# Performance work log

Hardware: AMD Instinct MI355X
Metric: run time of the kernel (lower is better)

## Reference

```python
import jax, jax.numpy as jnp
import numpy as np
import math

B, P = 4096, 512
WDT = 10          # lyr_wdt = number of irreps (multiplicity)
EPS2 = 1e-12      # NormActivation epsilon=1e-6, squared


def setup_inputs() -> dict:
    key = jax.random.key(0)
    ks = jax.random.split(key, 8)
    return {
        "invar_2b": jax.random.normal(ks[0], (B, P, 5), jnp.float32),
        "vectors_2b": jax.random.normal(ks[1], (B, P, 9), jnp.float32),
        # torch.nn.Linear params (stored as [in, out])
        "w1_0": jax.random.normal(ks[2], (5, WDT), jnp.float32) / math.sqrt(5.0),
        "b1_0": jnp.zeros((WDT,), jnp.float32),
        "w1_1": jax.random.normal(ks[3], (WDT, WDT), jnp.float32) / math.sqrt(float(WDT)),
        "b1_1": jnp.zeros((WDT,), jnp.float32),
        # o3.Linear weights (N(0,1) init, e3nn normalizes by sqrt(mul_in) in forward)
        "lin0_w": jax.random.normal(ks[4], (3, WDT), jnp.float32),
        "na0_b": jnp.zeros((WDT,), jnp.float32),   # NormActivation bias
        "lin1_w": jax.random.normal(ks[5], (WDT, WDT), jnp.float32),
        "na1_b": jnp.zeros((WDT,), jnp.float32),
        "final_w": jax.random.normal(ks[6], (WDT, 1), jnp.float32),
    }


def _self_intrc(x, w, bias):
    """o3.Linear (mul_in x 1o -> mul_out x 1o) + NormActivation(tanh, eps=1e-6, bias).

    x: [B, P, mul_in, 3]
    """
    mul_in = x.shape[-2]
    # single l=1 -> l=1 path; e3nn o3.Linear scales by 1/sqrt(fan_in)
    y = jnp.einsum('bpuc,uw->bpwc', x, w) / jnp.sqrt(jnp.float32(mul_in))
    # NormActivation: norm per irrep, clamped at eps^2 before sqrt
    n = jnp.sqrt(jnp.maximum(jnp.sum(y * y, axis=-1), EPS2))  # [B,P,mul_out]
    s = jnp.tanh(n + bias) / n                                # act(norm+b)/norm
    return y * s[..., None]


def reference(invar_2b, vectors_2b, w1_0, b1_0, w1_1, b1_1,
              lin0_w, na0_b, lin1_w, na1_b, final_w):
    # scalar branch: Linear(5,10) + ReLU, Linear(10,10) + ReLU
    y = jax.nn.relu(invar_2b @ w1_0 + b1_0)
    y = jax.nn.relu(y @ w1_1 + b1_1)              # [B, P, WDT] (10x0e)

    # equivariant branch: two self_intrc blocks on 3x1o -> 10x1o -> 10x1o
    v = vectors_2b.reshape(B, P, 3, 3)            # [B,P,3 irreps,3 comps]
    x = _self_intrc(v, lin0_w, na0_b)             # [B,P,WDT,3]
    x = _self_intrc(x, lin1_w, na1_b)             # [B,P,WDT,3]

    # ElementwiseTensorProduct(10x0e, 10x1o) -> 10x1o: per-irrep scalar gating
    x = y[..., None] * x                          # [B,P,WDT,3]

    # final o3.Linear 10x1o -> 1x1o
    x = jnp.einsum('bpuc,uw->bpwc', x, final_w) / jnp.sqrt(jnp.float32(WDT))
    return jnp.sum(x[..., 0, :], axis=1)          # sum over pairs -> [B, 3]
```

## Files before the change

kernel.cpp:

```cpp
#include <hip/hip_runtime.h>
#include <math.h>

#define BB 4096
#define PP 512
#define WDT 10

typedef float float2v __attribute__((ext_vector_type(2)));
typedef float float4v __attribute__((ext_vector_type(4)));

#define PKFMA(a, b, c) __builtin_elementwise_fma(a, b, c)
#define PKMAX(a, b)    __builtin_elementwise_max(a, b)

__device__ __forceinline__ float2v bc2(float s) { return (float2v){s, s}; }

__device__ __forceinline__ float fast_tanh(float x) {
    float e = __builtin_amdgcn_exp2f(x * 2.8853900817779268f);
    return 1.0f - 2.0f * __builtin_amdgcn_rcpf(e + 1.0f);
}

__global__ __launch_bounds__(512, 2) void frc_2b_kernel(
    const float* __restrict__ invar,
    const float* __restrict__ vectors,
    const float* __restrict__ w1_0,
    const float* __restrict__ b1_0,
    const float* __restrict__ w1_1,
    const float* __restrict__ b1_1,
    const float* __restrict__ lin0_w,
    const float* __restrict__ na0_b,
    const float* __restrict__ lin1_w,
    const float* __restrict__ na1_b,
    const float* __restrict__ final_w,
    float* __restrict__ out)
{
    __shared__ __align__(16) float wl[528];
    __shared__ float red[8][3];

    const int b   = blockIdx.x;
    const int tid = threadIdx.x;

    for (int t = tid; t < 528; t += 512) {
        float val = 0.f;
        if (t < 80) {
            int i = t >> 4, j = t & 15;
            if (j < WDT) val = w1_0[i * WDT + j];
        } else if (t < 240) {
            int u = t - 80, i = u >> 4, j = u & 15;
            if (j < WDT) val = w1_1[i * WDT + j];
        } else if (t < 288) {
            int u = t - 240, i = u >> 4, j = u & 15;
            if (j < WDT) val = lin0_w[i * WDT + j];
        } else if (t < 448) {
            int u = t - 288, i = u >> 4, j = u & 15;
            if (j < WDT) val = lin1_w[i * WDT + j];
        } else if (t < 464) {
            int u = t - 448; if (u < WDT) val = b1_0[u];
        } else if (t < 480) {
            int u = t - 464; if (u < WDT) val = b1_1[u];
        } else if (t < 496) {
            int u = t - 480; if (u < WDT) val = na0_b[u];
        } else if (t < 512) {
            int u = t - 496; if (u < WDT) val = na1_b[u];
        } else {
            int u = t - 512; if (u < WDT) val = final_w[u] * 0.31622776601683794f;
        }
        wl[t] = val;
    }

    const float* iv = invar   + ((size_t)b * PP + tid) * 5;
    const float* vv = vectors + ((size_t)b * PP + tid) * 9;
    float in5a[5];
    #pragma unroll
    for (int i = 0; i < 5; ++i) in5a[i] = iv[i];
    float v[9];
    #pragma unroll
    for (int i = 0; i < 9; ++i) v[i] = vv[i];

    __syncthreads();

    const float k3sq  = 0.33333333333333333f;
    const float k3k10 = 0.18257418583505536f;
    const float2v z2  = {0.f, 0.f};

    float2v yp[5];
    #pragma unroll
    for (int jp = 0; jp < 5; ++jp) yp[jp] = *(const float2v*)(wl + 448 + 2 * jp);
    #pragma unroll
    for (int i = 0; i < 5; ++i) {
        const float* r = wl + i * 16;
        float4v w03 = *(const float4v*)(r);
        float4v w47 = *(const float4v*)(r + 4);
        float2v w89 = *(const float2v*)(r + 8);
        float2v xb  = bc2(in5a[i]);
        yp[0] = PKFMA(__builtin_shufflevector(w03, w03, 0, 1), xb, yp[0]);
        yp[1] = PKFMA(__builtin_shufflevector(w03, w03, 2, 3), xb, yp[1]);
        yp[2] = PKFMA(__builtin_shufflevector(w47, w47, 0, 1), xb, yp[2]);
        yp[3] = PKFMA(__builtin_shufflevector(w47, w47, 2, 3), xb, yp[3]);
        yp[4] = PKFMA(w89, xb, yp[4]);
    }
    #pragma unroll
    for (int jp = 0; jp < 5; ++jp) yp[jp] = PKMAX(yp[jp], z2);

    float2v y2p[5];
    #pragma unroll
    for (int jp = 0; jp < 5; ++jp) y2p[jp] = *(const float2v*)(wl + 464 + 2 * jp);
    #pragma unroll
    for (int k = 0; k < WDT; ++k) {
        const float* r = wl + 80 + k * 16;
        float4v w03 = *(const float4v*)(r);
        float4v w47 = *(const float4v*)(r + 4);
        float2v w89 = *(const float2v*)(r + 8);
        float2v xb  = bc2(yp[k >> 1][k & 1]);
        y2p[0] = PKFMA(__builtin_shufflevector(w03, w03, 0, 1), xb, y2p[0]);
        y2p[1] = PKFMA(__builtin_shufflevector(w03, w03, 2, 3), xb, y2p[1]);
        y2p[2] = PKFMA(__builtin_shufflevector(w47, w47, 0, 1), xb, y2p[2]);
        y2p[3] = PKFMA(__builtin_shufflevector(w47, w47, 2, 3), xb, y2p[3]);
        y2p[4] = PKFMA(w89, xb, y2p[4]);
    }
    #pragma unroll
    for (int jp = 0; jp < 5; ++jp) y2p[jp] = PKMAX(y2p[jp], z2);

    float2v c0p[5], c1p[5], c2p[5];
    #pragma unroll
    for (int jp = 0; jp < 5; ++jp) { c0p[jp] = z2; c1p[jp] = z2; c2p[jp] = z2; }
    #pragma unroll
    for (int u = 0; u < 3; ++u) {
        const float* r = wl + 240 + u * 16;
        float4v w03 = *(const float4v*)(r);
        float4v w47 = *(const float4v*)(r + 4);
        float2v w89 = *(const float2v*)(r + 8);
        float2v wp[5] = {__builtin_shufflevector(w03, w03, 0, 1),
                         __builtin_shufflevector(w03, w03, 2, 3),
                         __builtin_shufflevector(w47, w47, 0, 1),
                         __builtin_shufflevector(w47, w47, 2, 3),
                         w89};
        float2v b0 = bc2(v[u * 3 + 0]), b1 = bc2(v[u * 3 + 1]), b2 = bc2(v[u * 3 + 2]);
        #pragma unroll
        for (int jp = 0; jp < 5; ++jp) {
            c0p[jp] = PKFMA(wp[jp], b0, c0p[jp]);
            c1p[jp] = PKFMA(wp[jp], b1, c1p[jp]);
            c2p[jp] = PKFMA(wp[jp], b2, c2p[jp]);
        }
    }
    float2v x0p[5], x1p[5], x2p[5];
    #pragma unroll
    for (int jp = 0; jp < 5; ++jp) {
        float2v n2p = PKFMA(c0p[jp], c0p[jp], PKFMA(c1p[jp], c1p[jp], c2p[jp] * c2p[jp]));
        float2v mp  = PKMAX(n2p * bc2(k3sq), bc2(1e-12f));
        float2v nab = *(const float2v*)(wl + 480 + 2 * jp);
        float fh[2];
        #pragma unroll
        for (int h = 0; h < 2; ++h) {
            float m     = mp[h];
            float inv_n = __builtin_amdgcn_rsqf(m);
            float n     = m * inv_n;
            float t     = fast_tanh(n + nab[h]);
            fh[h] = t * inv_n * k3k10;
        }
        float2v fp = {fh[0], fh[1]};
        x0p[jp] = c0p[jp] * fp;
        x1p[jp] = c1p[jp] * fp;
        x2p[jp] = c2p[jp] * fp;
    }

    float2v e0p[5], e1p[5], e2p[5];
    #pragma unroll
    for (int jp = 0; jp < 5; ++jp) { e0p[jp] = z2; e1p[jp] = z2; e2p[jp] = z2; }
    #pragma unroll
    for (int u = 0; u < WDT; ++u) {
        const float* r = wl + 288 + u * 16;
        float4v w03 = *(const float4v*)(r);
        float4v w47 = *(const float4v*)(r + 4);
        float2v w89 = *(const float2v*)(r + 8);
        float2v wp[5] = {__builtin_shufflevector(w03, w03, 0, 1),
                         __builtin_shufflevector(w03, w03, 2, 3),
                         __builtin_shufflevector(w47, w47, 0, 1),
                         __builtin_shufflevector(w47, w47, 2, 3),
                         w89};
        float2v b0 = bc2(x0p[u >> 1][u & 1]);
        float2v b1 = bc2(x1p[u >> 1][u & 1]);
        float2v b2 = bc2(x2p[u >> 1][u & 1]);
        #pragma unroll
        for (int jp = 0; jp < 5; ++jp) {
            e0p[jp] = PKFMA(wp[jp], b0, e0p[jp]);
            e1p[jp] = PKFMA(wp[jp], b1, e1p[jp]);
            e2p[jp] = PKFMA(wp[jp], b2, e2p[jp]);
        }
    }
    float2v a0p = z2, a1p = z2, a2p = z2;
    #pragma unroll
    for (int jp = 0; jp < 5; ++jp) {
        float2v n2p = PKFMA(e0p[jp], e0p[jp], PKFMA(e1p[jp], e1p[jp], e2p[jp] * e2p[jp]));
        float2v mp  = PKMAX(n2p, bc2(1e-12f));
        float2v nab = *(const float2v*)(wl + 496 + 2 * jp);
        float2v fwp = *(const float2v*)(wl + 512 + 2 * jp);
        float gh[2];
        #pragma unroll
        for (int h = 0; h < 2; ++h) {
            float m     = mp[h];
            float inv_n = __builtin_amdgcn_rsqf(m);
            float n     = m * inv_n;
            float t     = fast_tanh(n + nab[h]);
            gh[h] = y2p[jp][h] * t * inv_n * fwp[h];
        }
        float2v gp = {gh[0], gh[1]};
        a0p = PKFMA(e0p[jp], gp, a0p);
        a1p = PKFMA(e1p[jp], gp, a1p);
        a2p = PKFMA(e2p[jp], gp, a2p);
    }
    float acc0 = a0p[0] + a0p[1];
    float acc1 = a1p[0] + a1p[1];
    float acc2 = a2p[0] + a2p[1];

    #pragma unroll
    for (int off = 32; off > 0; off >>= 1) {
        acc0 += __shfl_down(acc0, off, 64);
        acc1 += __shfl_down(acc1, off, 64);
        acc2 += __shfl_down(acc2, off, 64);
    }
    const int wave = tid >> 6;
    if ((tid & 63) == 0) { red[wave][0] = acc0; red[wave][1] = acc1; red[wave][2] = acc2; }
    __syncthreads();
    if (tid == 0) {
        float r0 = 0.f, r1 = 0.f, r2 = 0.f;
        #pragma unroll
        for (int wv = 0; wv < 8; ++wv) { r0 += red[wv][0]; r1 += red[wv][1]; r2 += red[wv][2]; }
        out[b * 3 + 0] = r0;
        out[b * 3 + 1] = r1;
        out[b * 3 + 2] = r2;
    }
}

extern "C" void kernel_launch(void* const* d_in, const int* in_sizes, int n_in,
                              void* d_out, int out_size, void* d_ws, size_t ws_size,
                              hipStream_t stream) {
    const float* invar   = (const float*)d_in[0];
    const float* vectors = (const float*)d_in[1];
    const float* w1_0    = (const float*)d_in[2];
    const float* b1_0    = (const float*)d_in[3];
    const float* w1_1    = (const float*)d_in[4];
    const float* b1_1    = (const float*)d_in[5];
    const float* lin0_w  = (const float*)d_in[6];
    const float* na0_b   = (const float*)d_in[7];
    const float* lin1_w  = (const float*)d_in[8];
    const float* na1_b   = (const float*)d_in[9];
    const float* final_w = (const float*)d_in[10];
    float* out = (float*)d_out;

    frc_2b_kernel<<<BB, 512, 0, stream>>>(invar, vectors, w1_0, b1_0, w1_1, b1_1,
                                          lin0_w, na0_b, lin1_w, na1_b, final_w, out);
}
```

Baseline: 173.6 us.

## Read weights directly from global memory instead of staging them in LDS

```diff
diff --git a/kernel.cpp b/kernel.cpp
--- a/kernel.cpp
+++ b/kernel.cpp
@@ -6,10 +6,10 @@
 #define WDT 10
 
 typedef float float2v __attribute__((ext_vector_type(2)));
-typedef float float4v __attribute__((ext_vector_type(4)));
 
 #define PKFMA(a, b, c) __builtin_elementwise_fma(a, b, c)
 #define PKMAX(a, b)    __builtin_elementwise_max(a, b)
+#define FENCE()        __builtin_amdgcn_sched_barrier(0)
 
 __device__ __forceinline__ float2v bc2(float s) { return (float2v){s, s}; }
 
@@ -18,7 +18,7 @@
     return 1.0f - 2.0f * __builtin_amdgcn_rcpf(e + 1.0f);
 }
 
-__global__ __launch_bounds__(512, 2) void frc_2b_kernel(
+__global__ __launch_bounds__(512) void frc_2b_kernel(
     const float* __restrict__ invar,
     const float* __restrict__ vectors,
     const float* __restrict__ w1_0,
@@ -32,39 +32,10 @@
     const float* __restrict__ final_w,
     float* __restrict__ out)
 {
-    __shared__ __align__(16) float wl[528];
     __shared__ float red[8][3];
 
     const int b   = blockIdx.x;
     const int tid = threadIdx.x;
-
-    for (int t = tid; t < 528; t += 512) {
-        float val = 0.f;
-        if (t < 80) {
-            int i = t >> 4, j = t & 15;
-            if (j < WDT) val = w1_0[i * WDT + j];
-        } else if (t < 240) {
-            int u = t - 80, i = u >> 4, j = u & 15;
-            if (j < WDT) val = w1_1[i * WDT + j];
-        } else if (t < 288) {
-            int u = t - 240, i = u >> 4, j = u & 15;
-            if (j < WDT) val = lin0_w[i * WDT + j];
-        } else if (t < 448) {
-            int u = t - 288, i = u >> 4, j = u & 15;
-            if (j < WDT) val = lin1_w[i * WDT + j];
-        } else if (t < 464) {
-            int u = t - 448; if (u < WDT) val = b1_0[u];
-        } else if (t < 480) {
-            int u = t - 464; if (u < WDT) val = b1_1[u];
-        } else if (t < 496) {
-            int u = t - 480; if (u < WDT) val = na0_b[u];
-        } else if (t < 512) {
-            int u = t - 496; if (u < WDT) val = na1_b[u];
-        } else {
-            int u = t - 512; if (u < WDT) val = final_w[u] * 0.31622776601683794f;
-        }
-        wl[t] = val;
-    }
 
     const float* iv = invar   + ((size_t)b * PP + tid) * 5;
     const float* vv = vectors + ((size_t)b * PP + tid) * 9;
@@ -75,70 +46,67 @@
     #pragma unroll
     for (int i = 0; i < 9; ++i) v[i] = vv[i];
 
-    __syncthreads();
-
     const float k3sq  = 0.33333333333333333f;
     const float k3k10 = 0.18257418583505536f;
+    const float k10   = 0.31622776601683794f;
     const float2v z2  = {0.f, 0.f};
 
     float2v yp[5];
     #pragma unroll
-    for (int jp = 0; jp < 5; ++jp) yp[jp] = *(const float2v*)(wl + 448 + 2 * jp);
+    for (int jp = 0; jp < 5; ++jp) yp[jp] = *(const float2v*)(b1_0 + 2 * jp);
     #pragma unroll
     for (int i = 0; i < 5; ++i) {
-        const float* r = wl + i * 16;
-        float4v w03 = *(const float4v*)(r);
-        float4v w47 = *(const float4v*)(r + 4);
-        float2v w89 = *(const float2v*)(r + 8);
-        float2v xb  = bc2(in5a[i]);
-        yp[0] = PKFMA(__builtin_shufflevector(w03, w03, 0, 1), xb, yp[0]);
-        yp[1] = PKFMA(__builtin_shufflevector(w03, w03, 2, 3), xb, yp[1]);
-        yp[2] = PKFMA(__builtin_shufflevector(w47, w47, 0, 1), xb, yp[2]);
-        yp[3] = PKFMA(__builtin_shufflevector(w47, w47, 2, 3), xb, yp[3]);
-        yp[4] = PKFMA(w89, xb, yp[4]);
+        const float2v xb = bc2(in5a[i]);
+        #pragma unroll
+        for (int jp = 0; jp < 5; ++jp) {
+            float2v wp = *(const float2v*)(w1_0 + i * WDT + 2 * jp);
+            yp[jp] = PKFMA(wp, xb, yp[jp]);
+        }
     }
     #pragma unroll
     for (int jp = 0; jp < 5; ++jp) yp[jp] = PKMAX(yp[jp], z2);
+    FENCE();
 
     float2v y2p[5];
     #pragma unroll
-    for (int jp = 0; jp < 5; ++jp) y2p[jp] = *(const float2v*)(wl + 464 + 2 * jp);
-    #pragma unroll
-    for (int k = 0; k < WDT; ++k) {
-        const float* r = wl + 80 + k * 16;
-        float4v w03 = *(const float4v*)(r);
-        float4v w47 = *(const float4v*)(r + 4);
-        float2v w89 = *(const float2v*)(r + 8);
-        float2v xb  = bc2(yp[k >> 1][k & 1]);
-        y2p[0] = PKFMA(__builtin_shufflevector(w03, w03, 0, 1), xb, y2p[0]);
-        y2p[1] = PKFMA(__builtin_shufflevector(w03, w03, 2, 3), xb, y2p[1]);
-        y2p[2] = PKFMA(__builtin_shufflevector(w47, w47, 0, 1), xb, y2p[2]);
-        y2p[3] = PKFMA(__builtin_shufflevector(w47, w47, 2, 3), xb, y2p[3]);
-        y2p[4] = PKFMA(w89, xb, y2p[4]);
+    for (int jp = 0; jp < 5; ++jp) y2p[jp] = *(const float2v*)(b1_1 + 2 * jp);
+    #pragma unroll
+    for (int k = 0; k < 5; ++k) {
+        const float2v xb = bc2(yp[k >> 1][k & 1]);
+        #pragma unroll
+        for (int jp = 0; jp < 5; ++jp) {
+            float2v wp = *(const float2v*)(w1_1 + k * WDT + 2 * jp);
+            y2p[jp] = PKFMA(wp, xb, y2p[jp]);
+        }
+    }
+    FENCE();
+    #pragma unroll
+    for (int k = 5; k < WDT; ++k) {
+        const float2v xb = bc2(yp[k >> 1][k & 1]);
+        #pragma unroll
+        for (int jp = 0; jp < 5; ++jp) {
+            float2v wp = *(const float2v*)(w1_1 + k * WDT + 2 * jp);
+            y2p[jp] = PKFMA(wp, xb, y2p[jp]);
+        }
     }
     #pragma unroll
     for (int jp = 0; jp < 5; ++jp) y2p[jp] = PKMAX(y2p[jp], z2);
+    FENCE();
 
     float2v c0p[5], c1p[5], c2p[5];
     #pragma unroll
     for (int jp = 0; jp < 5; ++jp) { c0p[jp] = z2; c1p[jp] = z2; c2p[jp] = z2; }
     #pragma unroll
     for (int u = 0; u < 3; ++u) {
-        const float* r = wl + 240 + u * 16;
-        float4v w03 = *(const float4v*)(r);
-        float4v w47 = *(const float4v*)(r + 4);
-        float2v w89 = *(const float2v*)(r + 8);
-        float2v wp[5] = {__builtin_shufflevector(w03, w03, 0, 1),
-                         __builtin_shufflevector(w03, w03, 2, 3),
-                         __builtin_shufflevector(w47, w47, 0, 1),
-                         __builtin_shufflevector(w47, w47, 2, 3),
-                         w89};
-        float2v b0 = bc2(v[u * 3 + 0]), b1 = bc2(v[u * 3 + 1]), b2 = bc2(v[u * 3 + 2]);
-        #pragma unroll
-        for (int jp = 0; jp < 5; ++jp) {
-            c0p[jp] = PKFMA(wp[jp], b0, c0p[jp]);
-            c1p[jp] = PKFMA(wp[jp], b1, c1p[jp]);
-            c2p[jp] = PKFMA(wp[jp], b2, c2p[jp]);
+        const float2v b0 = bc2(v[u * 3 + 0]);
+        const float2v b1 = bc2(v[u * 3 + 1]);
+        const float2v b2 = bc2(v[u * 3 + 2]);
+        #pragma unroll
+        for (int jp = 0; jp < 5; ++jp) {
+            float2v wp = *(const float2v*)(lin0_w + u * WDT + 2 * jp);
+            c0p[jp] = PKFMA(wp, b0, c0p[jp]);
+            c1p[jp] = PKFMA(wp, b1, c1p[jp]);
+            c2p[jp] = PKFMA(wp, b2, c2p[jp]);
         }
     }
     float2v x0p[5], x1p[5], x2p[5];
@@ -146,7 +114,7 @@
     for (int jp = 0; jp < 5; ++jp) {
         float2v n2p = PKFMA(c0p[jp], c0p[jp], PKFMA(c1p[jp], c1p[jp], c2p[jp] * c2p[jp]));
         float2v mp  = PKMAX(n2p * bc2(k3sq), bc2(1e-12f));
-        float2v nab = *(const float2v*)(wl + 480 + 2 * jp);
+        float2v nab = *(const float2v*)(na0_b + 2 * jp);
         float fh[2];
         #pragma unroll
         for (int h = 0; h < 2; ++h) {
@@ -161,38 +129,47 @@
         x1p[jp] = c1p[jp] * fp;
         x2p[jp] = c2p[jp] * fp;
     }
+    FENCE();
 
     float2v e0p[5], e1p[5], e2p[5];
     #pragma unroll
     for (int jp = 0; jp < 5; ++jp) { e0p[jp] = z2; e1p[jp] = z2; e2p[jp] = z2; }
     #pragma unroll
-    for (int u = 0; u < WDT; ++u) {
-        const float* r = wl + 288 + u * 16;
-        float4v w03 = *(const float4v*)(r);
-        float4v w47 = *(const float4v*)(r + 4);
-        float2v w89 = *(const float2v*)(r + 8);
-        float2v wp[5] = {__builtin_shufflevector(w03, w03, 0, 1),
-                         __builtin_shufflevector(w03, w03, 2, 3),
-                         __builtin_shufflevector(w47, w47, 0, 1),
-                         __builtin_shufflevector(w47, w47, 2, 3),
-                         w89};
-        float2v b0 = bc2(x0p[u >> 1][u & 1]);
-        float2v b1 = bc2(x1p[u >> 1][u & 1]);
-        float2v b2 = bc2(x2p[u >> 1][u & 1]);
-        #pragma unroll
-        for (int jp = 0; jp < 5; ++jp) {
-            e0p[jp] = PKFMA(wp[jp], b0, e0p[jp]);
-            e1p[jp] = PKFMA(wp[jp], b1, e1p[jp]);
-            e2p[jp] = PKFMA(wp[jp], b2, e2p[jp]);
-        }
-    }
+    for (int u = 0; u < 5; ++u) {
+        const float2v b0 = bc2(x0p[u >> 1][u & 1]);
+        const float2v b1 = bc2(x1p[u >> 1][u & 1]);
+        const float2v b2 = bc2(x2p[u >> 1][u & 1]);
+        #pragma unroll
+        for (int jp = 0; jp < 5; ++jp) {
+            float2v wp = *(const float2v*)(lin1_w + u * WDT + 2 * jp);
+            e0p[jp] = PKFMA(wp, b0, e0p[jp]);
+            e1p[jp] = PKFMA(wp, b1, e1p[jp]);
+            e2p[jp] = PKFMA(wp, b2, e2p[jp]);
+        }
+    }
+    FENCE();
+    #pragma unroll
+    for (int u = 5; u < WDT; ++u) {
+        const float2v b0 = bc2(x0p[u >> 1][u & 1]);
+        const float2v b1 = bc2(x1p[u >> 1][u & 1]);
+        const float2v b2 = bc2(x2p[u >> 1][u & 1]);
+        #pragma unroll
+        for (int jp = 0; jp < 5; ++jp) {
+            float2v wp = *(const float2v*)(lin1_w + u * WDT + 2 * jp);
+            e0p[jp] = PKFMA(wp, b0, e0p[jp]);
+            e1p[jp] = PKFMA(wp, b1, e1p[jp]);
+            e2p[jp] = PKFMA(wp, b2, e2p[jp]);
+        }
+    }
+    FENCE();
+
     float2v a0p = z2, a1p = z2, a2p = z2;
     #pragma unroll
     for (int jp = 0; jp < 5; ++jp) {
         float2v n2p = PKFMA(e0p[jp], e0p[jp], PKFMA(e1p[jp], e1p[jp], e2p[jp] * e2p[jp]));
         float2v mp  = PKMAX(n2p, bc2(1e-12f));
-        float2v nab = *(const float2v*)(wl + 496 + 2 * jp);
-        float2v fwp = *(const float2v*)(wl + 512 + 2 * jp);
+        float2v nab = *(const float2v*)(na1_b + 2 * jp);
+        float2v fwp = *(const float2v*)(final_w + 2 * jp);
         float gh[2];
         #pragma unroll
         for (int h = 0; h < 2; ++h) {
@@ -207,9 +184,9 @@
         a1p = PKFMA(e1p[jp], gp, a1p);
         a2p = PKFMA(e2p[jp], gp, a2p);
     }
-    float acc0 = a0p[0] + a0p[1];
-    float acc1 = a1p[0] + a1p[1];
-    float acc2 = a2p[0] + a2p[1];
+    float acc0 = (a0p[0] + a0p[1]) * k10;
+    float acc1 = (a1p[0] + a1p[1]) * k10;
+    float acc2 = (a2p[0] + a2p[1]) * k10;
 
     #pragma unroll
     for (int off = 32; off > 0; off >>= 1) {
```

Result: faster. 165.8 us (-4.5%).
